# Optimization experiments

Measured on AMD Instinct MI355X. Metric: run time of the kernel, lower is better.

Reference implementation:

```python
import jax, jax.numpy as jnp
import numpy as np


def setup_inputs() -> dict:
    key = jax.random.key(0)
    k1, k2, k3, k4, k5 = jax.random.split(key, 5)
    B, S, K, N, G = 4, 2048, 4096, 4096, 64  # G = group_size -> num_groups = K // G = 64
    x = jax.random.normal(k1, (B, S, K), dtype=jnp.float32)
    # int2 codes stored one-per-int8 slot (low 2 bits valid); use int32 container
    weight_q = jax.random.randint(k2, (N, K), 0, 4, dtype=jnp.int32)
    scale = jax.random.uniform(k3, (N, K // G), dtype=jnp.float32) * 0.05 + 0.01
    zp = jax.random.uniform(k4, (N, K // G), dtype=jnp.float32) * 3.0
    bias = jax.random.normal(k5, (N,), dtype=jnp.float32)
    return {"x": x, "weight_q": weight_q, "scale": scale, "zp": zp, "bias": bias}


def _dequant(weight_q, scale, zp):
    # weight_q: [N, K] int codes in [0,4); scale/zp: [N, num_groups]
    N, K = weight_q.shape
    num_groups = scale.shape[1]
    gs = K // num_groups  # group_size
    q = weight_q.astype(jnp.float32).reshape(N, num_groups, gs)
    w = (q - zp[:, :, None]) * scale[:, :, None]
    return w.reshape(N, K)


def reference(x, weight_q, scale, zp, bias):
    # asymm_qw2_gemm: out = x @ dequant(W)^T + bias
    w = _dequant(weight_q, scale, zp)            # [N, K]
    out = jnp.einsum('bsk,nk->bsn', x, w)        # [B, S, N]
    return out + bias
```

## Files before the change

kernel.cpp:

```cpp
#include <hip/hip_runtime.h>
#include <stdint.h>


typedef __attribute__((ext_vector_type(4))) float  f32x4;
typedef __attribute__((ext_vector_type(4))) int    i32x4;
typedef __attribute__((ext_vector_type(8))) __bf16 bf16x8;
typedef __attribute__((ext_vector_type(8))) unsigned short u16x8;

__device__ __forceinline__ unsigned short f2bf(float f) {
  unsigned u = __builtin_bit_cast(unsigned, f);
  u += 0x7fffu + ((u >> 16) & 1u);
  return (unsigned short)(u >> 16);
}

__device__ __forceinline__ void async16(const void* g, void* l) {
  __builtin_amdgcn_global_load_lds(
      (const __attribute__((address_space(1))) unsigned int*)g,
      (__attribute__((address_space(3))) unsigned int*)l, 16, 0, 0);
}

__global__ __launch_bounds__(256) void prep_kernel(
    const float* __restrict__ x, unsigned short* __restrict__ xb, int xunits,
    const int* __restrict__ wq, const float* __restrict__ scale,
    const float* __restrict__ zp, unsigned short* __restrict__ wb,
    int wunits, int K, int G, int ng) {
  const int stride = gridDim.x * 256;
  const int i0 = blockIdx.x * 256 + threadIdx.x;
  for (int u = i0; u < xunits; u += stride) {
    const f32x4* xp = (const f32x4*)x + (size_t)u * 2;
    f32x4 a = xp[0], b = xp[1];
    u16x8 o;
    o[0] = f2bf(a[0]); o[1] = f2bf(a[1]); o[2] = f2bf(a[2]); o[3] = f2bf(a[3]);
    o[4] = f2bf(b[0]); o[5] = f2bf(b[1]); o[6] = f2bf(b[2]); o[7] = f2bf(b[3]);
    *((u16x8*)xb + u) = o;
  }
  for (int u = i0; u < wunits; u += stride) {
    int k8 = u * 8;
    int n = k8 / K, kk = k8 % K;
    int g = kk / G;
    float s  = scale[(size_t)n * ng + g];
    float bz = -zp[(size_t)n * ng + g] * s;
    const i32x4* wp = (const i32x4*)wq + (size_t)u * 2;
    i32x4 qa = wp[0], qb = wp[1];
    u16x8 o;
    o[0] = f2bf((float)qa[0] * s + bz); o[1] = f2bf((float)qa[1] * s + bz);
    o[2] = f2bf((float)qa[2] * s + bz); o[3] = f2bf((float)qa[3] * s + bz);
    o[4] = f2bf((float)qb[0] * s + bz); o[5] = f2bf((float)qb[1] * s + bz);
    o[6] = f2bf((float)qb[2] * s + bz); o[7] = f2bf((float)qb[3] * s + bz);
    *((u16x8*)wb + u) = o;
  }
}

#define BM 256
#define BN 256
#define TK 64
#define REG 8192

__global__ __launch_bounds__(512, 2) void gemm_bt_kernel(
    const unsigned short* __restrict__ A,
    const unsigned short* __restrict__ B,
    const float* __restrict__ bias,
    float* __restrict__ C, int M, int N, int K) {
  __shared__ unsigned short As[4 * REG];
  __shared__ unsigned short Bs[4 * REG];

  const int tid  = threadIdx.x;
  const int lane = tid & 63;
  const int wave = tid >> 6;
  const int wm = wave >> 2, wn = wave & 3;
  const int q = lane >> 4, r = lane & 15;

  int id = blockIdx.x;
  {
    int nwg = gridDim.x;
    if ((nwg & 7) == 0) id = (id & 7) * (nwg >> 3) + (id >> 3);
  }
  const int nbx = N / BN;
  const int m0 = (id / nbx) * BM;
  const int n0 = (id % nbx) * BN;

  const int srow = tid >> 2;
  const int gch  = (tid & 3) ^ ((tid >> 3) & 3);
  const unsigned short* aG = A + (size_t)(m0 + srow) * K + gch * 8;
  const unsigned short* bG = B + (size_t)(n0 + srow) * K + gch * 8;
  const size_t rb = (size_t)128 * K;

  unsigned short* aS = As + tid * 8;
  unsigned short* bS = Bs + tid * 8;

  const int qc8 = (q ^ ((r >> 1) & 3)) * 8;
  const unsigned short* aRd = As + (wm * 128 + r) * 32 + qc8;
  const unsigned short* bRd = Bs + (wn * 64  + r) * 32 + qc8;

  f32x4 acc[8][4] = {};
  const int NT = K / TK;

#define STG(S, G, par, kh, kk) { \
    unsigned short* l = (S) + ((par) * 2 + (kh)) * REG; \
    async16((G) + (kk) + (kh) * 32, l); \
    async16((G) + rb + (kk) + (kh) * 32, l + 4096); }

#define RD4(DST, PTR, O) \
    _Pragma("unroll") \
    for (int i_ = 0; i_ < 4; ++i_) \
      (DST)[i_] = *(const bf16x8*)&(PTR)[((O) + i_) * 512];

#define MF16(AF, BF, RO) \
    __builtin_amdgcn_s_setprio(1); \
    _Pragma("unroll") \
    for (int i_ = 0; i_ < 4; ++i_) \
      _Pragma("unroll") \
      for (int j_ = 0; j_ < 4; ++j_) \
        acc[(RO) + i_][j_] = __builtin_amdgcn_mfma_f32_16x16x32_bf16( \
            (AF)[i_], (BF)[j_], acc[(RO) + i_][j_], 0, 0, 0); \
    __builtin_amdgcn_s_setprio(0);

  bf16x8 afA[4], afB[4], bfP[4], bfQ[4];

  STG(aS, aG, 0, 0, 0) STG(bS, bG, 0, 0, 0)
  STG(aS, aG, 0, 1, 0) STG(bS, bG, 0, 1, 0)
  if (NT > 1) { STG(aS, aG, 1, 0, TK) STG(bS, bG, 1, 0, TK) }
  if (NT > 1) asm volatile("s_waitcnt vmcnt(4)" ::: "memory");
  else        asm volatile("s_waitcnt vmcnt(0)" ::: "memory");
  __builtin_amdgcn_s_barrier();
  RD4(afA, aRd, 0)
  RD4(bfP, bRd, 0)

#pragma unroll 1
  for (int t = 0; t < NT; ++t) {
    const int par = t & 1, nxt = par ^ 1;
    const bool pf = (t + 1 < NT);
    const int kk1 = (t + 1) * TK;
    const unsigned short* a0 = aRd + (par * 2 + 0) * REG;
    const unsigned short* a1 = aRd + (par * 2 + 1) * REG;
    const unsigned short* b1 = bRd + (par * 2 + 1) * REG;

    RD4(afB, a0, 4)
    MF16(afA, bfP, 0)

    if (pf) { STG(aS, aG, nxt, 1, kk1) STG(bS, bG, nxt, 1, kk1) }
    RD4(afA, a1, 0)
    RD4(bfQ, b1, 0)
    MF16(afB, bfP, 4)

    if (pf) asm volatile("s_waitcnt vmcnt(4) lgkmcnt(0)" ::: "memory");
    else    asm volatile("s_waitcnt vmcnt(0) lgkmcnt(0)" ::: "memory");
    __builtin_amdgcn_s_barrier();

    RD4(afB, a1, 4)
    MF16(afA, bfQ, 0)

    if (pf) {
      const unsigned short* na0 = aRd + (nxt * 2) * REG;
      const unsigned short* nb0 = bRd + (nxt * 2) * REG;
      RD4(afA, na0, 0)
      RD4(bfP, nb0, 0)
    }
    if (t + 2 < NT) {
      STG(aS, aG, par, 0, (t + 2) * TK) STG(bS, bG, par, 0, (t + 2) * TK)
    }
    MF16(afB, bfQ, 4)

    if (pf) {
      if (t + 2 < NT) asm volatile("s_waitcnt vmcnt(4) lgkmcnt(0)" ::: "memory");
      else            asm volatile("s_waitcnt vmcnt(0) lgkmcnt(0)" ::: "memory");
      __builtin_amdgcn_s_barrier();
    }
  }

  float bv[4];
#pragma unroll
  for (int j = 0; j < 4; ++j) bv[j] = bias[n0 + wn * 64 + j * 16 + r];
#pragma unroll
  for (int i = 0; i < 8; ++i) {
    int mbase = m0 + wm * 128 + i * 16 + q * 4;
#pragma unroll
    for (int e = 0; e < 4; ++e) {
      float* crow = C + (size_t)(mbase + e) * N + n0 + wn * 64 + r;
#pragma unroll
      for (int j = 0; j < 4; ++j)
        crow[j * 16] = acc[i][j][e] + bv[j];
    }
  }
}

__global__ __launch_bounds__(256) void naive_kernel(
    const float* __restrict__ x, const int* __restrict__ wq,
    const float* __restrict__ scale, const float* __restrict__ zp,
    const float* __restrict__ bias, float* __restrict__ out,
    int M, int N, int K, int G) {
  int idx = blockIdx.x * 256 + threadIdx.x;
  if (idx >= M * N) return;
  int m = idx / N, n = idx % N;
  const float* xr = x + (size_t)m * K;
  const int* wr = wq + (size_t)n * K;
  int ng = K / G;
  float acc = 0.f;
  for (int g = 0; g < ng; ++g) {
    float s = scale[(size_t)n * ng + g];
    float b = -zp[(size_t)n * ng + g] * s;
    for (int k = 0; k < G; ++k)
      acc += xr[g * G + k] * ((float)wr[g * G + k] * s + b);
  }
  out[idx] = acc + bias[n];
}

extern "C" void kernel_launch(void* const* d_in, const int* in_sizes, int n_in,
                              void* d_out, int out_size, void* d_ws, size_t ws_size,
                              hipStream_t stream) {
  const float* x     = (const float*)d_in[0];
  const int*   wq    = (const int*)d_in[1];
  const float* scale = (const float*)d_in[2];
  const float* zp    = (const float*)d_in[3];
  const float* bias  = (const float*)d_in[4];
  float* out = (float*)d_out;

  const int N  = in_sizes[4];
  const int K  = in_sizes[1] / N;
  const int ng = in_sizes[2] / N;
  const int G  = K / ng;
  const int M  = in_sizes[0] / K;

  size_t xb_bytes = (size_t)M * K * 2;
  size_t wb_bytes = (size_t)N * K * 2;
  bool divisible = (M % BM == 0) && (N % BN == 0) && (K % TK == 0) &&
                   (G % 8 == 0);
  if (ws_size < xb_bytes + wb_bytes || !divisible) {
    int total = M * N;
    naive_kernel<<<dim3((total + 255) / 256), dim3(256), 0, stream>>>(
        x, wq, scale, zp, bias, out, M, N, K, G);
    return;
  }

  unsigned short* xb = (unsigned short*)d_ws;
  unsigned short* wb = (unsigned short*)((char*)d_ws + xb_bytes);

  int xunits = M * K / 8;
  int wunits = N * K / 8;
  prep_kernel<<<dim3(2048), dim3(256), 0, stream>>>(
      x, xb, xunits, wq, scale, zp, wb, wunits, K, G, ng);

  dim3 grid((M / BM) * (N / BN));
  gemm_bt_kernel<<<grid, dim3(512), 0, stream>>>(xb, wb, bias, out, M, N, K);
}
```

Baseline: 558.3 us.

## Restructure GEMM main loop into four-phase ping-pong schedule with 64-wide swizzled LDS tiles

Reorganizes the bf16 GEMM's LDS layout from two 32-wide K halves into full 64-wide K rows with an XOR swizzle over 8 chunks. Each wave now loads its A and B fragments once per tile, and the K-tile is split into four MFMA phases separated by barriers. Global-to-LDS prefetch for the next tile is issued as A in phase 0 and B in phase 1, followed by a full vmcnt(0) wait at the end of each tile. The aim is a more regular, interleaved schedule of memory and MFMA work across waves. In exchange it adds more barriers per tile and drops the deeper prefetch the old loop kept in flight.

```diff
diff --git a/kernel.cpp b/kernel.cpp
--- a/kernel.cpp
+++ b/kernel.cpp
@@ -54,15 +54,15 @@
 #define BM 256
 #define BN 256
 #define TK 64
-#define REG 8192
+#define RSZ (128 * 64)
 
 __global__ __launch_bounds__(512, 2) void gemm_bt_kernel(
     const unsigned short* __restrict__ A,
     const unsigned short* __restrict__ B,
     const float* __restrict__ bias,
     float* __restrict__ C, int M, int N, int K) {
-  __shared__ unsigned short As[4 * REG];
-  __shared__ unsigned short Bs[4 * REG];
+  __shared__ unsigned short As[4 * RSZ];
+  __shared__ unsigned short Bs[4 * RSZ];
 
   const int tid  = threadIdx.x;
   const int lane = tid & 63;
@@ -79,92 +79,115 @@
   const int m0 = (id / nbx) * BM;
   const int n0 = (id % nbx) * BN;
 
-  const int srow = tid >> 2;
-  const int gch  = (tid & 3) ^ ((tid >> 3) & 3);
-  const unsigned short* aG = A + (size_t)(m0 + srow) * K + gch * 8;
-  const unsigned short* bG = B + (size_t)(n0 + srow) * K + gch * 8;
-  const size_t rb = (size_t)128 * K;
-
-  unsigned short* aS = As + tid * 8;
-  unsigned short* bS = Bs + tid * 8;
-
-  const int qc8 = (q ^ ((r >> 1) & 3)) * 8;
-  const unsigned short* aRd = As + (wm * 128 + r) * 32 + qc8;
-  const unsigned short* bRd = Bs + (wn * 64  + r) * 32 + qc8;
+  const int wgA = wave & 3;
+  const int bh  = wn >> 1;
+  const int wgB = (wave & 1) | ((wave >> 2) << 1);
+  const int lr8 = lane >> 3;
+  const int gc  = (lane & 7) ^ (lr8 & 7);
+  const unsigned short* aGbase =
+      A + (size_t)(m0 + wm * 128 + wgA * 32 + lr8) * K + gc * 8;
+  const unsigned short* bGbase =
+      B + (size_t)(n0 + bh * 128 + wgB * 32 + lr8) * K + gc * 8;
+
+#define STG_A(np, kk) { \
+    unsigned short* d = As + ((np) * 2 + wm) * RSZ + wgA * 2048 + (lane << 3); \
+    const unsigned short* g = aGbase + (kk); \
+    async16(g,                  d);        \
+    async16(g +  8 * (size_t)K, d +  512); \
+    async16(g + 16 * (size_t)K, d + 1024); \
+    async16(g + 24 * (size_t)K, d + 1536); }
+
+#define STG_B(np, kk) { \
+    unsigned short* d = Bs + ((np) * 2 + bh) * RSZ + wgB * 2048 + (lane << 3); \
+    const unsigned short* g = bGbase + (kk); \
+    async16(g,                  d);        \
+    async16(g +  8 * (size_t)K, d +  512); \
+    async16(g + 16 * (size_t)K, d + 1024); \
+    async16(g + 24 * (size_t)K, d + 1536); }
+
+  const int key  = r & 7;
+  const int cho0 = ((q) ^ key) * 8;
+  const int cho1 = ((4 + q) ^ key) * 8;
+  const int aoff0 = r * 64 + cho0, aoff1 = r * 64 + cho1;
+  const int boff0 = ((wn & 1) * 64 + r) * 64 + cho0;
+  const int boff1 = ((wn & 1) * 64 + r) * 64 + cho1;
 
   f32x4 acc[8][4] = {};
   const int NT = K / TK;
 
-#define STG(S, G, par, kh, kk) { \
-    unsigned short* l = (S) + ((par) * 2 + (kh)) * REG; \
-    async16((G) + (kk) + (kh) * 32, l); \
-    async16((G) + rb + (kk) + (kh) * 32, l + 4096); }
-
-#define RD4(DST, PTR, O) \
-    _Pragma("unroll") \
-    for (int i_ = 0; i_ < 4; ++i_) \
-      (DST)[i_] = *(const bf16x8*)&(PTR)[((O) + i_) * 512];
-
-#define MF16(AF, BF, RO) \
-    __builtin_amdgcn_s_setprio(1); \
-    _Pragma("unroll") \
-    for (int i_ = 0; i_ < 4; ++i_) \
-      _Pragma("unroll") \
-      for (int j_ = 0; j_ < 4; ++j_) \
-        acc[(RO) + i_][j_] = __builtin_amdgcn_mfma_f32_16x16x32_bf16( \
-            (AF)[i_], (BF)[j_], acc[(RO) + i_][j_], 0, 0, 0); \
-    __builtin_amdgcn_s_setprio(0);
-
-  bf16x8 afA[4], afB[4], bfP[4], bfQ[4];
-
-  STG(aS, aG, 0, 0, 0) STG(bS, bG, 0, 0, 0)
-  STG(aS, aG, 0, 1, 0) STG(bS, bG, 0, 1, 0)
-  if (NT > 1) { STG(aS, aG, 1, 0, TK) STG(bS, bG, 1, 0, TK) }
-  if (NT > 1) asm volatile("s_waitcnt vmcnt(4)" ::: "memory");
-  else        asm volatile("s_waitcnt vmcnt(0)" ::: "memory");
+  STG_A(0, 0) STG_B(0, 0)
+  asm volatile("s_waitcnt vmcnt(0)" ::: "memory");
   __builtin_amdgcn_s_barrier();
-  RD4(afA, aRd, 0)
-  RD4(bfP, bRd, 0)
+  asm volatile("" ::: "memory");
 
 #pragma unroll 1
   for (int t = 0; t < NT; ++t) {
-    const int par = t & 1, nxt = par ^ 1;
+    const int par = t & 1, np = par ^ 1;
     const bool pf = (t + 1 < NT);
     const int kk1 = (t + 1) * TK;
-    const unsigned short* a0 = aRd + (par * 2 + 0) * REG;
-    const unsigned short* a1 = aRd + (par * 2 + 1) * REG;
-    const unsigned short* b1 = bRd + (par * 2 + 1) * REG;
-
-    RD4(afB, a0, 4)
-    MF16(afA, bfP, 0)
-
-    if (pf) { STG(aS, aG, nxt, 1, kk1) STG(bS, bG, nxt, 1, kk1) }
-    RD4(afA, a1, 0)
-    RD4(bfQ, b1, 0)
-    MF16(afB, bfP, 4)
-
-    if (pf) asm volatile("s_waitcnt vmcnt(4) lgkmcnt(0)" ::: "memory");
-    else    asm volatile("s_waitcnt vmcnt(0) lgkmcnt(0)" ::: "memory");
-    __builtin_amdgcn_s_barrier();
-
-    RD4(afB, a1, 4)
-    MF16(afA, bfQ, 0)
-
-    if (pf) {
-      const unsigned short* na0 = aRd + (nxt * 2) * REG;
-      const unsigned short* nb0 = bRd + (nxt * 2) * REG;
-      RD4(afA, na0, 0)
-      RD4(bfP, nb0, 0)
+    const unsigned short* Ar = As + (par * 2 + wm) * RSZ;
+    const unsigned short* Br = Bs + (par * 2 + bh) * RSZ;
+
+    bf16x8 bb0[4], bb1[4];
+
+    {
+      bf16x8 aa0[2], aa1[2];
+#pragma unroll
+      for (int nj = 0; nj < 4; ++nj) {
+        bb0[nj] = *(const bf16x8*)&Br[nj * 1024 + boff0];
+        bb1[nj] = *(const bf16x8*)&Br[nj * 1024 + boff1];
+      }
+#pragma unroll
+      for (int m2 = 0; m2 < 2; ++m2) {
+        aa0[m2] = *(const bf16x8*)&Ar[m2 * 1024 + aoff0];
+        aa1[m2] = *(const bf16x8*)&Ar[m2 * 1024 + aoff1];
+      }
+      if (pf) STG_A(np, kk1)
+      asm volatile("s_waitcnt lgkmcnt(8)" ::: "memory");
+      __builtin_amdgcn_s_barrier();
+      asm volatile("s_waitcnt lgkmcnt(0)" ::: "memory");
+      __builtin_amdgcn_s_setprio(1);
+#pragma unroll
+      for (int m2 = 0; m2 < 2; ++m2)
+#pragma unroll
+        for (int nj = 0; nj < 4; ++nj) {
+          acc[m2][nj] = __builtin_amdgcn_mfma_f32_16x16x32_bf16(
+              aa0[m2], bb0[nj], acc[m2][nj], 0, 0, 0);
+          acc[m2][nj] = __builtin_amdgcn_mfma_f32_16x16x32_bf16(
+              aa1[m2], bb1[nj], acc[m2][nj], 0, 0, 0);
+        }
+      __builtin_amdgcn_s_setprio(0);
+      asm volatile("" ::: "memory");
+      __builtin_amdgcn_s_barrier();
+      asm volatile("" ::: "memory");
     }
-    if (t + 2 < NT) {
-      STG(aS, aG, par, 0, (t + 2) * TK) STG(bS, bG, par, 0, (t + 2) * TK)
-    }
-    MF16(afB, bfQ, 4)
-
-    if (pf) {
-      if (t + 2 < NT) asm volatile("s_waitcnt vmcnt(4) lgkmcnt(0)" ::: "memory");
-      else            asm volatile("s_waitcnt vmcnt(0) lgkmcnt(0)" ::: "memory");
-      __builtin_amdgcn_s_barrier();
+
+#pragma unroll
+    for (int p = 1; p < 4; ++p) {
+      bf16x8 aa0[2], aa1[2];
+#pragma unroll
+      for (int m2 = 0; m2 < 2; ++m2) {
+        aa0[m2] = *(const bf16x8*)&Ar[(2 * p + m2) * 1024 + aoff0];
+        aa1[m2] = *(const bf16x8*)&Ar[(2 * p + m2) * 1024 + aoff1];
+      }
+      if (p == 1 && pf) STG_B(np, kk1)
+      __builtin_amdgcn_s_barrier();
+      asm volatile("s_waitcnt lgkmcnt(0)" ::: "memory");
+      __builtin_amdgcn_s_setprio(1);
+#pragma unroll
+      for (int m2 = 0; m2 < 2; ++m2)
+#pragma unroll
+        for (int nj = 0; nj < 4; ++nj) {
+          acc[2 * p + m2][nj] = __builtin_amdgcn_mfma_f32_16x16x32_bf16(
+              aa0[m2], bb0[nj], acc[2 * p + m2][nj], 0, 0, 0);
+          acc[2 * p + m2][nj] = __builtin_amdgcn_mfma_f32_16x16x32_bf16(
+              aa1[m2], bb1[nj], acc[2 * p + m2][nj], 0, 0, 0);
+        }
+      __builtin_amdgcn_s_setprio(0);
+      asm volatile("" ::: "memory");
+      if (p == 3) asm volatile("s_waitcnt vmcnt(0)" ::: "memory");
+      __builtin_amdgcn_s_barrier();
+      asm volatile("" ::: "memory");
     }
   }
 
```

Measured after the change: 531.5 us. 4.8% less time.
